# Kernel tuning notes

Hardware: AMD Instinct MI355X
Metric: run time of the kernel (lower is better)

## Reference

```python
import jax, jax.numpy as jnp
import numpy as np

N = 65536          # nodes
E = 1_048_576      # edges (avg degree 16)
IN_DIM = 16        # input_irreps = 16x0e
OUT_DIM = 8        # output_irreps = 8x0e
S_MUL = 32         # hidden 0e multiplicity
V_MUL = 16         # hidden 1o multiplicity
HID = S_MUL + 3 * V_MUL  # 80
LAYERS = 3
DEG = 16.0


def fctp(feat, eattr, w1, w2, w3, w4):
    """FullyConnectedTensorProduct(hidden x '1x0e+1x1o' -> hidden) per edge.
    Paths: 0e*0e->0e, 1o*1o->0e (dot, CG 1/sqrt(3)), 0e*1o->1o, 1o*0e->1o.
    Path weights mix multiplicities; e3nn-style fan-in normalization."""
    s1 = feat[:, :S_MUL]                         # [E, 32]
    v1 = feat[:, S_MUL:].reshape(-1, V_MUL, 3)   # [E, 16, 3]
    s2 = eattr[:, 0]                             # [E]
    v2 = eattr[:, 1:4]                           # [E, 3]
    c = 1.0 / np.sqrt(2.0)  # two paths per output irrep
    out_s = c * (jnp.einsum('ea,e,ac->ec', s1, s2, w1) / np.sqrt(S_MUL)
                 + jnp.einsum('eak,ek,ac->ec', v1, v2, w2) / np.sqrt(3.0 * V_MUL))
    out_v = c * (jnp.einsum('ea,ek,ac->eck', s1, v2, w3) / np.sqrt(S_MUL)
                 + jnp.einsum('eak,e,ac->eck', v1, s2, w4) / np.sqrt(V_MUL))
    return jnp.concatenate([out_s, out_v.reshape(-1, 3 * V_MUL)], axis=-1)


def setup_inputs() -> dict:
    key = jax.random.key(0)
    ks = jax.random.split(key, 12)
    inp = {
        'x': jax.random.normal(ks[0], (N, IN_DIM), jnp.float32),
        'edge_index': jax.random.randint(ks[1], (2, E), 0, N, jnp.int64 if jax.config.jax_enable_x64 else jnp.int32),
        'edge_attr': jax.random.normal(ks[2], (E, 4), jnp.float32),
        'W_in': jax.random.normal(ks[3], (IN_DIM, HID), jnp.float32) / np.sqrt(IN_DIM),
        'b_in': jnp.zeros((HID,), jnp.float32),
        'tp_w1': jax.random.normal(ks[4], (LAYERS, S_MUL, S_MUL), jnp.float32),
        'tp_w2': jax.random.normal(ks[5], (LAYERS, V_MUL, S_MUL), jnp.float32),
        'tp_w3': jax.random.normal(ks[6], (LAYERS, S_MUL, V_MUL), jnp.float32),
        'tp_w4': jax.random.normal(ks[7], (LAYERS, V_MUL, V_MUL), jnp.float32),
        'W_out': jax.random.normal(ks[8], (HID, OUT_DIM), jnp.float32) / np.sqrt(HID),
        'b_out': jnp.zeros((OUT_DIM,), jnp.float32),
    }
    return inp


def reference(x, edge_index, edge_attr, W_in, b_in, tp_w1, tp_w2, tp_w3, tp_w4, W_out, b_out):
    src, dst = edge_index[0], edge_index[1]
    h = x @ W_in + b_in                                   # [N, 80]
    for l in range(LAYERS):
        m = fctp(h[src], edge_attr, tp_w1[l], tp_w2[l], tp_w3[l], tp_w4[l])  # [E, 80]
        h = jax.ops.segment_sum(m, dst, num_segments=N) / np.sqrt(DEG)       # [N, 80]
    h = jax.nn.relu(h)
    return h @ W_out + b_out                              # [N, 8]
```

## Files before the change

kernel.cpp:

```cpp
#include <hip/hip_runtime.h>

#define NN 65536
#define NE 1048576
#define HID 80

typedef unsigned int u32;
typedef unsigned short u16;
typedef unsigned long long u64;

typedef float v4f __attribute__((ext_vector_type(4)));

__device__ __forceinline__ u16 f2bf(float f) {
  u32 u = __float_as_uint(f);
  u = (u + 0x7fffu + ((u >> 16) & 1u)) >> 16;
  return (u16)u;
}
__device__ __forceinline__ float bfhi(u32 packed) {
  return __uint_as_float(packed & 0xffff0000u);
}
__device__ __forceinline__ float bflo(u32 packed) {
  return __uint_as_float(packed << 16);
}
__device__ __forceinline__ float4 ntload4f(const float4* p) {
  v4f v = __builtin_nontemporal_load((const v4f*)p);
  return make_float4(v.x, v.y, v.z, v.w);
}
__device__ __forceinline__ int ntloadi(const int* p) {
  return __builtin_nontemporal_load(p);
}

__global__ __launch_bounds__(256) void k_hist_in(const int* __restrict__ dst,
    int* __restrict__ counts, int* __restrict__ rank, int* __restrict__ dcnt,
    const float* __restrict__ x, const float* __restrict__ W,
    const float* __restrict__ b, u16* __restrict__ hmain,
    u16* __restrict__ htail) {
  if (blockIdx.x < 512) {
    if (blockIdx.x == 0 && threadIdx.x < 16) dcnt[threadIdx.x] = 0;
    int base = blockIdx.x * 2048 + threadIdx.x;
#pragma unroll
    for (int k = 0; k < 8; k++) {
      int idx = base + k * 256;
      rank[idx] = atomicAdd(&counts[ntloadi(dst + idx)], 1);
    }
  } else {
    int idx = (blockIdx.x - 512) * 256 + threadIdx.x;
    if (idx >= NN * 10) return;
    int n = idx / 10, part = idx % 10;
    const float4* xr = (const float4*)(x + (size_t)n * 16);
    float4 x0 = xr[0], x1 = xr[1], x2 = xr[2], x3 = xr[3];
    const float xs[16] = {x0.x, x0.y, x0.z, x0.w, x1.x, x1.y, x1.z, x1.w,
                          x2.x, x2.y, x2.z, x2.w, x3.x, x3.y, x3.z, x3.w};
    float acc[8];
#pragma unroll
    for (int j = 0; j < 8; j++) acc[j] = b[part * 8 + j];
#pragma unroll
    for (int k = 0; k < 16; k++) {
#pragma unroll
      for (int j = 0; j < 8; j++) acc[j] += xs[k] * W[k * HID + part * 8 + j];
    }
    u32 p0 = (u32)f2bf(acc[0]) | ((u32)f2bf(acc[1]) << 16);
    u32 p1 = (u32)f2bf(acc[2]) | ((u32)f2bf(acc[3]) << 16);
    u32 p2 = (u32)f2bf(acc[4]) | ((u32)f2bf(acc[5]) << 16);
    u32 p3 = (u32)f2bf(acc[6]) | ((u32)f2bf(acc[7]) << 16);
    uint4 vv = make_uint4(p0, p1, p2, p3);
    if (part < 8)
      *(uint4*)(hmain + (size_t)n * 64 + part * 8) = vv;
    else
      *(uint4*)(htail + (size_t)n * 16 + (part - 8) * 8) = vv;
  }
}

__global__ __launch_bounds__(256) void k_nb_scan(const int* __restrict__ counts,
    int* __restrict__ offsets, int* __restrict__ blocksum,
    int* __restrict__ dcnt, int* __restrict__ brank, int* __restrict__ bidx) {
  __shared__ int sc[256];
  int t = threadIdx.x;
  if (blockIdx.x < 64) {
    int base = blockIdx.x * 1024 + t * 4;
    int p0 = (counts[base] + 7) & ~7;
    int p1 = (counts[base + 1] + 7) & ~7;
    int p2 = (counts[base + 2] + 7) & ~7;
    int p3 = (counts[base + 3] + 7) & ~7;
    int s = p0 + p1 + p2 + p3;
    sc[t] = s;
    __syncthreads();
    for (int d = 1; d < 256; d <<= 1) {
      int v = (t >= d) ? sc[t - d] : 0;
      __syncthreads();
      sc[t] += v;
      __syncthreads();
    }
    int excl = sc[t] - s;
    offsets[base] = excl;
    offsets[base + 1] = excl + p0;
    offsets[base + 2] = excl + p0 + p1;
    offsets[base + 3] = excl + p0 + p1 + p2;
    if (t == 255) blocksum[blockIdx.x] = sc[255];
  } else {
    int n = (blockIdx.x - 64) * 256 + t;
    int degp = (counts[n] + 7) & ~7;
    int b = 15 - min(degp >> 3, 15);
    int lane = t & 63;
    int base = 0;
#pragma unroll 1
    for (int bb = 0; bb < 16; bb++) {
      u64 m = __ballot(b == bb);
      if (b == bb) {
        int leader = __ffsll((long long)m) - 1;
        int lr = __popcll(m & ((lane == 63) ? ~0ull >> 1 : ((1ull << lane) - 1)));
        int bs = 0;
        if (lane == leader) bs = atomicAdd(&dcnt[bb], __popcll(m));
        bs = __shfl(bs, leader, 64);
        base = bs + lr;
      }
    }
    brank[n] = base;
    bidx[n] = b;
  }
}

__global__ __launch_bounds__(256) void k_fill_fin(const int* __restrict__ src,
    const int* __restrict__ dst, const float4* __restrict__ eattr,
    const int* __restrict__ offsets, const int* __restrict__ blocksum,
    const int* __restrict__ rank, uint4* __restrict__ erec,
    const int* __restrict__ counts, const int* __restrict__ dcnt,
    const int* __restrict__ brank, const int* __restrict__ bidx,
    int* __restrict__ nperm, int* __restrict__ offs_fin) {
  __shared__ int bsum[64];
  __shared__ int dsum[16];
  int t = threadIdx.x;
  if (t < 64) {
    int v = blocksum[t];
    int incl = v;
#pragma unroll
    for (int d = 1; d < 64; d <<= 1) {
      int o = __shfl_up(incl, d, 64);
      if (t >= d) incl += o;
    }
    bsum[t] = incl - v;
  } else if (t < 80) {
    int l = t - 64;
    int v = dcnt[l];
    int incl = v;
#pragma unroll
    for (int d = 1; d < 16; d <<= 1) {
      int o = __shfl_up(incl, d, 64);
      if (l >= d) incl += o;
    }
    dsum[l] = incl - v;
  }
  __syncthreads();

  if (blockIdx.x < 512) {
    int base = blockIdx.x * 2048 + t;
#pragma unroll
    for (int k = 0; k < 8; k++) {
      int idx = base + k * 256;
      int d = ntloadi(dst + idx);
      float4 ea = ntload4f(eattr + idx);
      int s = ntloadi(src + idx);
      u32 c01 = (u32)f2bf(ea.x) | ((u32)f2bf(ea.y) << 16);
      u32 c23 = (u32)f2bf(ea.z) | ((u32)f2bf(ea.w) << 16);
      int pos = offsets[d] + bsum[d >> 10] + rank[idx];
      erec[pos] = make_uint4((u32)s, c01, c23, 0u);
    }
  } else {
    int n = (blockIdx.x - 512) * 256 + t;
    int off = offsets[n] + bsum[n >> 10];
    offs_fin[n] = off;
    int deg = counts[n];
    int degp = (deg + 7) & ~7;
    uint4 z = make_uint4(0u, 0u, 0u, 0u);
    for (int e = deg; e < degp; e++) erec[off + e] = z;
    nperm[dsum[bidx[n]] + brank[n]] = n;
  }
}

template <int LAST>
__global__ __launch_bounds__(128, 3) void k_msg(const u16* __restrict__ hmain,
    const u16* __restrict__ htail, u16* __restrict__ omain,
    u16* __restrict__ otail,
    const float* __restrict__ w1, const float* __restrict__ w2,
    const float* __restrict__ w3, const float* __restrict__ w4,
    const int* __restrict__ offsets, const int* __restrict__ counts,
    const int* __restrict__ nperm, const uint4* __restrict__ erec,
    const float* __restrict__ Wout, const float* __restrict__ bout,
    float* __restrict__ outp) {
  __shared__ float Rlds[8][4][81];
  int tid = threadIdx.x;
  const int q = tid >> 4;
  const int c = tid & 15;
  const int n = nperm[blockIdx.x * 8 + q];

  float R[4][5];
#pragma unroll
  for (int j = 0; j < 4; j++)
#pragma unroll
    for (int i = 0; i < 5; i++) R[j][i] = 0.f;

  const int start = offsets[n];
  const int degp = (counts[n] + 7) & ~7;
  const int B = degp >> 3;
  const uint2* hrow = (const uint2*)hmain + c;
  const u16* trow = htail + c;

  int i = 0;
  for (; i + 2 <= B; i += 2) {
    const int baseA = start + 8 * i;
    const int baseB = baseA + 8;
    uint4 rA[8], rB[8];
#pragma unroll
    for (int k = 0; k < 8; k++) rA[k] = erec[baseA + k];
#pragma unroll
    for (int k = 0; k < 8; k++) rB[k] = erec[baseB + k];
    uint2 hA[8], hB[8];
    u32 tA[8], tB[8];
#pragma unroll
    for (int k = 0; k < 8; k++) {
      size_t s16 = (size_t)rA[k].x * 16;
      hA[k] = hrow[s16];
      tA[k] = trow[s16];
    }
#pragma unroll
    for (int k = 0; k < 8; k++) {
      size_t s16 = (size_t)rB[k].x * 16;
      hB[k] = hrow[s16];
      tB[k] = trow[s16];
    }
#pragma unroll
    for (int k = 0; k < 8; k++) {
      float A0 = bflo(hA[k].x), A1 = bfhi(hA[k].x);
      float A2 = bflo(hA[k].y), A3 = bfhi(hA[k].y);
      float A4 = bflo(tA[k]);
      float f0 = bflo(rA[k].y), f1 = bfhi(rA[k].y);
      float f2 = bflo(rA[k].z), f3 = bfhi(rA[k].z);
      R[0][0] += f0 * A0; R[0][1] += f0 * A1; R[0][2] += f0 * A2;
      R[0][3] += f0 * A3; R[0][4] += f0 * A4;
      R[1][0] += f1 * A0; R[1][1] += f1 * A1; R[1][2] += f1 * A2;
      R[1][3] += f1 * A3; R[1][4] += f1 * A4;
      R[2][0] += f2 * A0; R[2][1] += f2 * A1; R[2][2] += f2 * A2;
      R[2][3] += f2 * A3; R[2][4] += f2 * A4;
      R[3][0] += f3 * A0; R[3][1] += f3 * A1; R[3][2] += f3 * A2;
      R[3][3] += f3 * A3; R[3][4] += f3 * A4;
    }
#pragma unroll
    for (int k = 0; k < 8; k++) {
      float A0 = bflo(hB[k].x), A1 = bfhi(hB[k].x);
      float A2 = bflo(hB[k].y), A3 = bfhi(hB[k].y);
      float A4 = bflo(tB[k]);
      float f0 = bflo(rB[k].y), f1 = bfhi(rB[k].y);
      float f2 = bflo(rB[k].z), f3 = bfhi(rB[k].z);
      R[0][0] += f0 * A0; R[0][1] += f0 * A1; R[0][2] += f0 * A2;
      R[0][3] += f0 * A3; R[0][4] += f0 * A4;
      R[1][0] += f1 * A0; R[1][1] += f1 * A1; R[1][2] += f1 * A2;
      R[1][3] += f1 * A3; R[1][4] += f1 * A4;
      R[2][0] += f2 * A0; R[2][1] += f2 * A1; R[2][2] += f2 * A2;
      R[2][3] += f2 * A3; R[2][4] += f2 * A4;
      R[3][0] += f3 * A0; R[3][1] += f3 * A1; R[3][2] += f3 * A2;
      R[3][3] += f3 * A3; R[3][4] += f3 * A4;
    }
  }
  if (i < B) {
    const int baseA = start + 8 * i;
    uint4 rA[8];
#pragma unroll
    for (int k = 0; k < 8; k++) rA[k] = erec[baseA + k];
    uint2 hA[8];
    u32 tA[8];
#pragma unroll
    for (int k = 0; k < 8; k++) {
      size_t s16 = (size_t)rA[k].x * 16;
      hA[k] = hrow[s16];
      tA[k] = trow[s16];
    }
#pragma unroll
    for (int k = 0; k < 8; k++) {
      float A0 = bflo(hA[k].x), A1 = bfhi(hA[k].x);
      float A2 = bflo(hA[k].y), A3 = bfhi(hA[k].y);
      float A4 = bflo(tA[k]);
      float f0 = bflo(rA[k].y), f1 = bfhi(rA[k].y);
      float f2 = bflo(rA[k].z), f3 = bfhi(rA[k].z);
      R[0][0] += f0 * A0; R[0][1] += f0 * A1; R[0][2] += f0 * A2;
      R[0][3] += f0 * A3; R[0][4] += f0 * A4;
      R[1][0] += f1 * A0; R[1][1] += f1 * A1; R[1][2] += f1 * A2;
      R[1][3] += f1 * A3; R[1][4] += f1 * A4;
      R[2][0] += f2 * A0; R[2][1] += f2 * A1; R[2][2] += f2 * A2;
      R[2][3] += f2 * A3; R[2][4] += f2 * A4;
      R[3][0] += f3 * A0; R[3][1] += f3 * A1; R[3][2] += f3 * A2;
      R[3][3] += f3 * A3; R[3][4] += f3 * A4;
    }
  }

#pragma unroll
  for (int j = 0; j < 4; j++) {
#pragma unroll
    for (int k = 0; k < 4; k++) Rlds[q][j][4 * c + k] = R[j][k];
    Rlds[q][j][64 + c] = R[j][4];
  }

  const float C1 = 0.03125f;
  const float C2 = 0.025515518f;
  const float C3 = 0.03125f;
  const float C4 = 0.044194174f;

  u16* opm = omain + (size_t)n * 64;

  float s0 = 0.f, s1 = 0.f;
#pragma unroll
  for (int a = 0; a < 32; a++) {
    float rs = Rlds[q][0][a];
    s0 += rs * w1[a * 32 + c];
    s1 += rs * w1[a * 32 + c + 16];
  }
  float t0 = 0.f, t1 = 0.f;
#pragma unroll
  for (int a = 0; a < 16; a++) {
    float T = Rlds[q][1][32 + 3 * a] + Rlds[q][2][33 + 3 * a] +
              Rlds[q][3][34 + 3 * a];
    t0 += T * w2[a * 32 + c];
    t1 += T * w2[a * 32 + c + 16];
  }

  float y[8];
  if (LAST) {
#pragma unroll
    for (int j = 0; j < 8; j++) y[j] = 0.f;
    float vs0 = C1 * s0 + C2 * t0;
    float vs1 = C1 * s1 + C2 * t1;
    vs0 = vs0 > 0.f ? vs0 : 0.f;
    vs1 = vs1 > 0.f ? vs1 : 0.f;
#pragma unroll
    for (int j = 0; j < 8; j++)
      y[j] += vs0 * Wout[c * 8 + j] + vs1 * Wout[(c + 16) * 8 + j];
  } else {
    opm[c] = f2bf(C1 * s0 + C2 * t0);
    opm[c + 16] = f2bf(C1 * s1 + C2 * t1);
  }

#pragma unroll
  for (int v2 = 0; v2 < 3; v2++) {
    int c2 = 32 + 16 * v2 + c;
    int cv = (c2 - 32) / 3, k = (c2 - 32) % 3;
    float a3 = 0.f, a4 = 0.f;
#pragma unroll
    for (int a = 0; a < 32; a++) a3 += Rlds[q][k + 1][a] * w3[a * 16 + cv];
#pragma unroll
    for (int a = 0; a < 16; a++)
      a4 += Rlds[q][0][32 + 3 * a + k] * w4[a * 16 + cv];
    float val = C3 * a3 + C4 * a4;
    if (LAST) {
      val = val > 0.f ? val : 0.f;
#pragma unroll
      for (int j = 0; j < 8; j++) y[j] += val * Wout[c2 * 8 + j];
    } else {
      u16 v = f2bf(val);
      if (v2 < 2) opm[32 + 16 * v2 + c] = v;
      else otail[(size_t)n * 16 + c] = v;
    }
  }

  if (LAST) {
#pragma unroll
    for (int m = 1; m <= 8; m <<= 1) {
#pragma unroll
      for (int j = 0; j < 8; j++) y[j] += __shfl_xor(y[j], m, 64);
    }
    float w = y[0];
#pragma unroll
    for (int j = 1; j < 8; j++)
      if (c == j) w = y[j];
    if (c < 8) outp[(size_t)n * 8 + c] = w + bout[c];
  }
}

extern "C" void kernel_launch(void* const* d_in, const int* in_sizes, int n_in,
                              void* d_out, int out_size, void* d_ws,
                              size_t ws_size, hipStream_t stream) {
  const float* x = (const float*)d_in[0];
  const int* ei = (const int*)d_in[1];
  const float* eattr = (const float*)d_in[2];
  const float* W_in = (const float*)d_in[3];
  const float* b_in = (const float*)d_in[4];
  const float* tp_w1 = (const float*)d_in[5];
  const float* tp_w2 = (const float*)d_in[6];
  const float* tp_w3 = (const float*)d_in[7];
  const float* tp_w4 = (const float*)d_in[8];
  const float* W_out = (const float*)d_in[9];
  const float* b_out = (const float*)d_in[10];
  float* out = (float*)d_out;

  char* ws = (char*)d_ws;
  size_t off = 0;
  auto alloc = [&](size_t bytes) {
    void* p = ws + off;
    off += (bytes + 255) & ~size_t(255);
    return p;
  };
  const size_t NEP = (size_t)NE + 8 * (size_t)NN;
  u16* hm_a = (u16*)alloc((size_t)NN * 64 * 2);
  u16* ht_a = (u16*)alloc((size_t)NN * 16 * 2);
  u16* hm_b = (u16*)alloc((size_t)NN * 64 * 2);
  u16* ht_b = (u16*)alloc((size_t)NN * 16 * 2);
  int* counts = (int*)alloc((size_t)NN * 4);
  int* offsets = (int*)alloc((size_t)NN * 4);
  int* offs_fin = (int*)alloc((size_t)NN * 4);
  int* blocksum = (int*)alloc(64 * 4);
  int* rank = (int*)alloc((size_t)NE * 4);
  int* dcnt = (int*)alloc(16 * 4);
  int* brank = (int*)alloc((size_t)NN * 4);
  int* bidx = (int*)alloc((size_t)NN * 4);
  int* nperm = (int*)alloc((size_t)NN * 4);
  uint4* erec = (uint4*)alloc(NEP * 16);

  const int* src = ei;
  const int* dst = ei + NE;

  hipMemsetAsync(counts, 0, (size_t)NN * 4, stream);
  k_hist_in<<<512 + (NN * 10 + 255) / 256, 256, 0, stream>>>(
      dst, counts, rank, dcnt, x, W_in, b_in, hm_a, ht_a);
  k_nb_scan<<<64 + NN / 256, 256, 0, stream>>>(counts, offsets, blocksum, dcnt,
                                               brank, bidx);
  k_fill_fin<<<512 + NN / 256, 256, 0, stream>>>(
      src, dst, (const float4*)eattr, offsets, blocksum, rank, erec, counts,
      dcnt, brank, bidx, nperm, offs_fin);

  u16* hmi = hm_a;
  u16* hti = ht_a;
  u16* hmo = hm_b;
  u16* hto = ht_b;
  for (int l = 0; l < 2; l++) {
    k_msg<0><<<NN / 8, 128, 0, stream>>>(hmi, hti, hmo, hto, tp_w1 + l * 1024,
                                         tp_w2 + l * 512, tp_w3 + l * 512,
                                         tp_w4 + l * 256, offs_fin, counts,
                                         nperm, erec, W_out, b_out, out);
    u16* t;
    t = hmi; hmi = hmo; hmo = t;
    t = hti; hti = hto; hto = t;
  }
  k_msg<1><<<NN / 8, 128, 0, stream>>>(hmi, hti, hmo, hto, tp_w1 + 2048,
                                       tp_w2 + 1024, tp_w3 + 1024, tp_w4 + 512,
                                       offs_fin, counts, nperm, erec,
                                       W_out, b_out, out);
}
```

Baseline: 386.8 us.

## Replace global-atomic counting sort of edges with two-pass bucketed radix partition

The edge CSR build changes from per-edge global atomics on 65536 node counters plus a scattered write into a two-pass radix scheme. First each block groups its edges by the high byte of dst in shared memory and writes them to 256 fixed-capacity buckets. Then one block per bucket builds local histograms, offsets and the final placement with shared-memory atomics. This avoids contended global atomics, the rank array and random global scatters, but adds an extra kernel, a 32MB temp buffer and a fixed bucket capacity (CAP=8192) that assumes a roughly uniform dst distribution.

```diff
diff --git a/kernel.cpp b/kernel.cpp
--- a/kernel.cpp
+++ b/kernel.cpp
@@ -3,6 +3,7 @@
 #define NN 65536
 #define NE 1048576
 #define HID 80
+#define CAP 8192
 
 typedef unsigned int u32;
 typedef unsigned short u16;
@@ -29,18 +30,63 @@
   return __builtin_nontemporal_load(p);
 }
 
-__global__ __launch_bounds__(256) void k_hist_in(const int* __restrict__ dst,
-    int* __restrict__ counts, int* __restrict__ rank, int* __restrict__ dcnt,
+__global__ __launch_bounds__(256) void k_p1_in(const int* __restrict__ dst,
+    const int* __restrict__ src, const float4* __restrict__ eattr,
+    int* __restrict__ bcnt, uint4* __restrict__ tmp,
     const float* __restrict__ x, const float* __restrict__ W,
     const float* __restrict__ b, u16* __restrict__ hmain,
     u16* __restrict__ htail) {
   if (blockIdx.x < 512) {
-    if (blockIdx.x == 0 && threadIdx.x < 16) dcnt[threadIdx.x] = 0;
-    int base = blockIdx.x * 2048 + threadIdx.x;
+    __shared__ int hist[256];
+    __shared__ int lofs[257];
+    __shared__ int gbase[256];
+    __shared__ int sc[256];
+    __shared__ uint4 buf[2048];
+    int t = threadIdx.x;
+    hist[t] = 0;
+    __syncthreads();
+    uint4 rec[8];
+    int bk[8], lr[8];
+    int base = blockIdx.x * 2048 + t;
 #pragma unroll
     for (int k = 0; k < 8; k++) {
       int idx = base + k * 256;
-      rank[idx] = atomicAdd(&counts[ntloadi(dst + idx)], 1);
+      int d = ntloadi(dst + idx);
+      float4 ea = ntload4f(eattr + idx);
+      int s = ntloadi(src + idx);
+      u32 c01 = (u32)f2bf(ea.x) | ((u32)f2bf(ea.y) << 16);
+      u32 c23 = (u32)f2bf(ea.z) | ((u32)f2bf(ea.w) << 16);
+      rec[k] = make_uint4((u32)s, c01, c23, (u32)d);
+      bk[k] = d >> 8;
+      lr[k] = atomicAdd(&hist[bk[k]], 1);
+    }
+    __syncthreads();
+    int h = hist[t];
+    gbase[t] = atomicAdd(&bcnt[t], h);
+    sc[t] = h;
+    __syncthreads();
+    for (int d = 1; d < 256; d <<= 1) {
+      int v = (t >= d) ? sc[t - d] : 0;
+      __syncthreads();
+      sc[t] += v;
+      __syncthreads();
+    }
+    lofs[t] = sc[t] - h;
+    if (t == 255) lofs[256] = 2048;
+    __syncthreads();
+#pragma unroll
+    for (int k = 0; k < 8; k++) buf[lofs[bk[k]] + lr[k]] = rec[k];
+    __syncthreads();
+#pragma unroll
+    for (int k = 0; k < 8; k++) {
+      int j = t + k * 256;
+      int lo = 0, hi = 256;
+      while (hi - lo > 1) {
+        int mid = (lo + hi) >> 1;
+        if (lofs[mid] <= j) lo = mid;
+        else hi = mid;
+      }
+      tmp[(size_t)lo * CAP + gbase[lo] + (j - lofs[lo])] = buf[j];
     }
   } else {
     int idx = (blockIdx.x - 512) * 256 + threadIdx.x;
@@ -70,42 +116,90 @@
   }
 }
 
-__global__ __launch_bounds__(256) void k_nb_scan(const int* __restrict__ counts,
-    int* __restrict__ offsets, int* __restrict__ blocksum,
-    int* __restrict__ dcnt, int* __restrict__ brank, int* __restrict__ bidx) {
+__global__ __launch_bounds__(256) void k_p15(const int* __restrict__ bcnt,
+    const uint4* __restrict__ tmp, int* __restrict__ counts_tot,
+    int* __restrict__ offsets, int* __restrict__ bucketsum) {
+  __shared__ int hist[256];
   __shared__ int sc[256];
   int t = threadIdx.x;
-  if (blockIdx.x < 64) {
-    int base = blockIdx.x * 1024 + t * 4;
-    int p0 = (counts[base] + 7) & ~7;
-    int p1 = (counts[base + 1] + 7) & ~7;
-    int p2 = (counts[base + 2] + 7) & ~7;
-    int p3 = (counts[base + 3] + 7) & ~7;
-    int s = p0 + p1 + p2 + p3;
-    sc[t] = s;
-    __syncthreads();
-    for (int d = 1; d < 256; d <<= 1) {
-      int v = (t >= d) ? sc[t - d] : 0;
-      __syncthreads();
-      sc[t] += v;
-      __syncthreads();
-    }
-    int excl = sc[t] - s;
-    offsets[base] = excl;
-    offsets[base + 1] = excl + p0;
-    offsets[base + 2] = excl + p0 + p1;
-    offsets[base + 3] = excl + p0 + p1 + p2;
-    if (t == 255) blocksum[blockIdx.x] = sc[255];
+  int b = blockIdx.x;
+  hist[t] = 0;
+  __syncthreads();
+  int cnt = bcnt[b];
+  const int* tw = (const int*)(tmp + (size_t)b * CAP);
+  for (int j = t; j < cnt; j += 256) atomicAdd(&hist[tw[j * 4 + 3] & 255], 1);
+  __syncthreads();
+  int deg = hist[t];
+  int p = (deg + 7) & ~7;
+  sc[t] = p;
+  __syncthreads();
+  for (int d = 1; d < 256; d <<= 1) {
+    int v = (t >= d) ? sc[t - d] : 0;
+    __syncthreads();
+    sc[t] += v;
+    __syncthreads();
+  }
+  counts_tot[b * 256 + t] = deg;
+  offsets[b * 256 + t] = sc[t] - p;
+  if (t == 255) bucketsum[b] = sc[255];
+}
+
+__global__ __launch_bounds__(256) void k_p2(const int* __restrict__ bcnt,
+    const uint4* __restrict__ tmp, const int* __restrict__ offsets,
+    const int* __restrict__ bucketsum, const int* __restrict__ counts_tot,
+    uint4* __restrict__ erec, int* __restrict__ offs_fin,
+    int* __restrict__ brank, int* __restrict__ bidx, int* __restrict__ dcnt) {
+  int t = threadIdx.x;
+  if (blockIdx.x < 256) {
+    __shared__ int bsum[256];
+    __shared__ int cur[256];
+    __shared__ int noff[256];
+    if (t < 64) {
+      int v0 = bucketsum[t * 4], v1 = bucketsum[t * 4 + 1];
+      int v2 = bucketsum[t * 4 + 2], v3 = bucketsum[t * 4 + 3];
+      int s = v0 + v1 + v2 + v3;
+      int incl = s;
+#pragma unroll
+      for (int d = 1; d < 64; d <<= 1) {
+        int o = __shfl_up(incl, d, 64);
+        if (t >= d) incl += o;
+      }
+      int base = incl - s;
+      bsum[t * 4] = base;
+      bsum[t * 4 + 1] = base + v0;
+      bsum[t * 4 + 2] = base + v0 + v1;
+      bsum[t * 4 + 3] = base + v0 + v1 + v2;
+    }
+    cur[t] = 0;
+    __syncthreads();
+    int b = blockIdx.x;
+    int off = offsets[b * 256 + t] + bsum[b];
+    noff[t] = off;
+    offs_fin[b * 256 + t] = off;
+    __syncthreads();
+    int cnt = bcnt[b];
+    const uint4* tb = tmp + (size_t)b * CAP;
+    for (int j = t; j < cnt; j += 256) {
+      uint4 r = tb[j];
+      int i = r.w & 255;
+      int lr = atomicAdd(&cur[i], 1);
+      erec[noff[i] + lr] = make_uint4(r.x, r.y, r.z, 0u);
+    }
+    __syncthreads();
+    int deg = cur[t];
+    int degp = (deg + 7) & ~7;
+    uint4 z = make_uint4(0u, 0u, 0u, 0u);
+    for (int e = deg; e < degp; e++) erec[noff[t] + e] = z;
   } else {
-    int n = (blockIdx.x - 64) * 256 + t;
-    int degp = (counts[n] + 7) & ~7;
-    int b = 15 - min(degp >> 3, 15);
+    int n = (blockIdx.x - 256) * 256 + t;
+    int degp = (counts_tot[n] + 7) & ~7;
+    int bb2 = 15 - min(degp >> 3, 15);
     int lane = t & 63;
     int base = 0;
 #pragma unroll 1
     for (int bb = 0; bb < 16; bb++) {
-      u64 m = __ballot(b == bb);
-      if (b == bb) {
+      u64 m = __ballot(bb2 == bb);
+      if (bb2 == bb) {
         int leader = __ffsll((long long)m) - 1;
         int lr = __popcll(m & ((lane == 63) ? ~0ull >> 1 : ((1ull << lane) - 1)));
         int bs = 0;
@@ -115,65 +209,28 @@
       }
     }
     brank[n] = base;
-    bidx[n] = b;
-  }
-}
-
-__global__ __launch_bounds__(256) void k_fill_fin(const int* __restrict__ src,
-    const int* __restrict__ dst, const float4* __restrict__ eattr,
-    const int* __restrict__ offsets, const int* __restrict__ blocksum,
-    const int* __restrict__ rank, uint4* __restrict__ erec,
-    const int* __restrict__ counts, const int* __restrict__ dcnt,
+    bidx[n] = bb2;
+  }
+}
+
+__global__ __launch_bounds__(256) void k_p3(const int* __restrict__ dcnt,
     const int* __restrict__ brank, const int* __restrict__ bidx,
-    int* __restrict__ nperm, int* __restrict__ offs_fin) {
-  __shared__ int bsum[64];
+    int* __restrict__ nperm) {
   __shared__ int dsum[16];
   int t = threadIdx.x;
-  if (t < 64) {
-    int v = blocksum[t];
+  if (t < 16) {
+    int v = dcnt[t];
     int incl = v;
 #pragma unroll
-    for (int d = 1; d < 64; d <<= 1) {
+    for (int d = 1; d < 16; d <<= 1) {
       int o = __shfl_up(incl, d, 64);
       if (t >= d) incl += o;
     }
-    bsum[t] = incl - v;
-  } else if (t < 80) {
-    int l = t - 64;
-    int v = dcnt[l];
-    int incl = v;
-#pragma unroll
-    for (int d = 1; d < 16; d <<= 1) {
-      int o = __shfl_up(incl, d, 64);
-      if (l >= d) incl += o;
-    }
-    dsum[l] = incl - v;
+    dsum[t] = incl - v;
   }
   __syncthreads();
-
-  if (blockIdx.x < 512) {
-    int base = blockIdx.x * 2048 + t;
-#pragma unroll
-    for (int k = 0; k < 8; k++) {
-      int idx = base + k * 256;
-      int d = ntloadi(dst + idx);
-      float4 ea = ntload4f(eattr + idx);
-      int s = ntloadi(src + idx);
-      u32 c01 = (u32)f2bf(ea.x) | ((u32)f2bf(ea.y) << 16);
-      u32 c23 = (u32)f2bf(ea.z) | ((u32)f2bf(ea.w) << 16);
-      int pos = offsets[d] + bsum[d >> 10] + rank[idx];
-      erec[pos] = make_uint4((u32)s, c01, c23, 0u);
-    }
-  } else {
-    int n = (blockIdx.x - 512) * 256 + t;
-    int off = offsets[n] + bsum[n >> 10];
-    offs_fin[n] = off;
-    int deg = counts[n];
-    int degp = (deg + 7) & ~7;
-    uint4 z = make_uint4(0u, 0u, 0u, 0u);
-    for (int e = deg; e < degp; e++) erec[off + e] = z;
-    nperm[dsum[bidx[n]] + brank[n]] = n;
-  }
+  int n = blockIdx.x * 256 + t;
+  nperm[dsum[bidx[n]] + brank[n]] = n;
 }
 
 template <int LAST>
@@ -401,28 +458,28 @@
   u16* ht_a = (u16*)alloc((size_t)NN * 16 * 2);
   u16* hm_b = (u16*)alloc((size_t)NN * 64 * 2);
   u16* ht_b = (u16*)alloc((size_t)NN * 16 * 2);
-  int* counts = (int*)alloc((size_t)NN * 4);
+  int* bcnt = (int*)alloc(256 * 4);
+  int* dcnt = (int*)alloc(16 * 4);
+  int* counts_tot = (int*)alloc((size_t)NN * 4);
   int* offsets = (int*)alloc((size_t)NN * 4);
   int* offs_fin = (int*)alloc((size_t)NN * 4);
-  int* blocksum = (int*)alloc(64 * 4);
-  int* rank = (int*)alloc((size_t)NE * 4);
-  int* dcnt = (int*)alloc(16 * 4);
+  int* bucketsum = (int*)alloc(256 * 4);
   int* brank = (int*)alloc((size_t)NN * 4);
   int* bidx = (int*)alloc((size_t)NN * 4);
   int* nperm = (int*)alloc((size_t)NN * 4);
+  uint4* tmp = (uint4*)alloc((size_t)256 * CAP * 16);
   uint4* erec = (uint4*)alloc(NEP * 16);
 
   const int* src = ei;
   const int* dst = ei + NE;
 
-  hipMemsetAsync(counts, 0, (size_t)NN * 4, stream);
-  k_hist_in<<<512 + (NN * 10 + 255) / 256, 256, 0, stream>>>(
-      dst, counts, rank, dcnt, x, W_in, b_in, hm_a, ht_a);
-  k_nb_scan<<<64 + NN / 256, 256, 0, stream>>>(counts, offsets, blocksum, dcnt,
-                                               brank, bidx);
-  k_fill_fin<<<512 + NN / 256, 256, 0, stream>>>(
-      src, dst, (const float4*)eattr, offsets, blocksum, rank, erec, counts,
-      dcnt, brank, bidx, nperm, offs_fin);
+  hipMemsetAsync(bcnt, 0, 1024 + 256, stream);
+  k_p1_in<<<512 + (NN * 10 + 255) / 256, 256, 0, stream>>>(
+      dst, src, (const float4*)eattr, bcnt, tmp, x, W_in, b_in, hm_a, ht_a);
+  k_p15<<<256, 256, 0, stream>>>(bcnt, tmp, counts_tot, offsets, bucketsum);
+  k_p2<<<512, 256, 0, stream>>>(bcnt, tmp, offsets, bucketsum, counts_tot,
+                                erec, offs_fin, brank, bidx, dcnt);
+  k_p3<<<256, 256, 0, stream>>>(dcnt, brank, bidx, nperm);
 
   u16* hmi = hm_a;
   u16* hti = ht_a;
@@ -431,7 +488,7 @@
   for (int l = 0; l < 2; l++) {
     k_msg<0><<<NN / 8, 128, 0, stream>>>(hmi, hti, hmo, hto, tp_w1 + l * 1024,
                                          tp_w2 + l * 512, tp_w3 + l * 512,
-                                         tp_w4 + l * 256, offs_fin, counts,
+                                         tp_w4 + l * 256, offs_fin, counts_tot,
                                          nperm, erec, W_out, b_out, out);
     u16* t;
     t = hmi; hmi = hmo; hmo = t;
@@ -439,6 +496,6 @@
   }
   k_msg<1><<<NN / 8, 128, 0, stream>>>(hmi, hti, hmo, hto, tp_w1 + 2048,
                                        tp_w2 + 1024, tp_w3 + 1024, tp_w4 + 512,
-                                       offs_fin, counts, nperm, erec,
+                                       offs_fin, counts_tot, nperm, erec,
                                        W_out, b_out, out);
 }
```

After: 344.1 us. 1.12x faster.
